# Kernel optimization log

Measured on AMD Instinct MI355X. Metric: run time of the kernel, lower is better.

Reference implementation:

```python
import jax, jax.numpy as jnp
import numpy as np

IN_DIM, UNITS, OUT_DIM = 128, 256, 8
DENSITY = 0.5  # 1 - sparsity_level
B, T = 256, 512


def _ncp_dims():
    Nm = OUT_DIM
    Nc = max(int(0.4 * (UNITS - Nm)), 1)   # command neurons (AutoNCP rule)
    Ni = UNITS - Nm - Nc                    # inter neurons
    return Ni, Nc, Nm


def _fanout_mask(rng, n_src, n_dst, fanout):
    # each source connects to `fanout` distinct random destinations
    idx = np.argsort(rng.random((n_src, n_dst)), axis=1)[:, :fanout]
    m = np.zeros((n_src, n_dst), dtype=np.int32)
    m[np.arange(n_src)[:, None], idx] = 1
    return m


def setup_inputs() -> dict:
    key = jax.random.key(0)
    rng = np.random.default_rng(22222)
    Ni, Nc, Nm = _ncp_dims()
    s_fan = max(int(Ni * DENSITY), 1)       # sensory fanout
    i_fan = max(int(Nc * DENSITY), 1)       # inter fanout
    m_fanin = max(int(Nc * DENSITY), 1)     # motor fanin
    M_si = _fanout_mask(rng, IN_DIM, Ni, s_fan)      # sensory -> inter
    M_ic = _fanout_mask(rng, Ni, Nc, i_fan)          # inter -> command
    M_cm = _fanout_mask(rng, Nm, Nc, m_fanin).T      # command -> motor (fanin per motor)

    def layer_mask(M_in, hid):
        # WiredCfCCell: concat input sparsity with dense ones for the recurrent block, then transpose
        return np.concatenate([M_in, np.ones((hid, hid), np.int32)], axis=0).T

    masks = [layer_mask(M_si, Ni), layer_mask(M_ic, Nc), layer_mask(M_cm, Nm)]
    dims = [(IN_DIM, Ni), (Ni, Nc), (Nc, Nm)]
    inp = {}
    for l, (fin, hid) in enumerate(dims):
        cat = fin + hid
        scale = 1.0 / np.sqrt(cat)
        for nm in ("w1", "w2", "wa", "wb"):
            inp[f"{nm}_{l}"] = jnp.asarray(rng.normal(0.0, scale, (hid, cat)).astype(np.float32))
        for nm in ("b1", "b2", "ba", "bb"):
            inp[f"{nm}_{l}"] = jnp.zeros((hid,), jnp.float32)
        inp[f"m{l}"] = jnp.asarray(masks[l])  # int32, constant sparsity mask
    k1, k2 = jax.random.split(key)
    inp["x"] = jax.random.normal(k1, (B, T, IN_DIM), jnp.float32)
    inp["dt"] = jax.random.uniform(k2, (1,), jnp.float32, 0.5, 1.5)
    return inp


def _cfc_cell(xh, w1, b1, w2, b2, wa, ba, wb, bb, m, ts):
    # CfCCell, mode='default', no backbone, sparsity mask on ff1/ff2 weights
    mf = m.astype(w1.dtype)
    ff1 = jnp.tanh(xh @ (w1 * mf).T + b1)
    ff2 = jnp.tanh(xh @ (w2 * mf).T + b2)
    t_interp = jax.nn.sigmoid((xh @ wa.T + ba) * ts + (xh @ wb.T + bb))
    return ff1 * (1.0 - t_interp) + t_interp * ff2


def _forward(x, dt, params, masks):
    Ni, Nc, Nm = _ncp_dims()
    ts = dt[0]
    h0 = jnp.zeros((x.shape[0], Ni), x.dtype)
    h1 = jnp.zeros((x.shape[0], Nc), x.dtype)
    h2 = jnp.zeros((x.shape[0], Nm), x.dtype)
    p0, p1, p2 = params

    def step(carry, xt):
        h0, h1, h2 = carry
        nh0 = _cfc_cell(jnp.concatenate([xt, h0], 1), *p0, masks[0], ts)
        nh1 = _cfc_cell(jnp.concatenate([nh0, h1], 1), *p1, masks[1], ts)
        nh2 = _cfc_cell(jnp.concatenate([nh1, h2], 1), *p2, masks[2], ts)
        return (nh0, nh1, nh2), nh2

    (h0, h1, h2), ys = jax.lax.scan(step, (h0, h1, h2), jnp.swapaxes(x, 0, 1))
    y = jnp.tanh(jnp.swapaxes(ys, 0, 1))          # (B, T, OUT_DIM), tanh output saturation
    h_out = jnp.concatenate([h0, h1, h2], axis=1)  # (B, units)
    return y, h_out


def reference(x, dt,
              w1_0, b1_0, w2_0, b2_0, wa_0, ba_0, wb_0, bb_0, m0,
              w1_1, b1_1, w2_1, b2_1, wa_1, ba_1, wb_1, bb_1, m1,
              w1_2, b1_2, w2_2, b2_2, wa_2, ba_2, wb_2, bb_2, m2):
    params = ((w1_0, b1_0, w2_0, b2_0, wa_0, ba_0, wb_0, bb_0),
              (w1_1, b1_1, w2_1, b2_1, wa_1, ba_1, wb_1, bb_1),
              (w1_2, b1_2, w2_2, b2_2, wa_2, ba_2, wb_2, bb_2))
    return _forward(x, dt, params, (m0, m1, m2))
```

## Files before the change

kernel.cpp:

```cpp
#include <hip/hip_runtime.h>
#include <cmath>


typedef _Float16 f16;
typedef f16 h4 __attribute__((ext_vector_type(4)));
typedef f16 h8 __attribute__((ext_vector_type(8)));
typedef float f4 __attribute__((ext_vector_type(4)));

#define MFMA(a, b, c) __builtin_amdgcn_mfma_f32_16x16x32_f16(a, b, c, 0, 0, 0)
#define RAW_BAR() asm volatile("s_waitcnt lgkmcnt(0)\n\ts_barrier" ::: "memory")

constexpr int IN_DIM = 128, Ni = 149, Nc = 99, Nm = 8;
constexpr int CAT0 = 277, CAT1 = 248, CAT2 = 107;
constexpr int Bsz = 256, Tsz = 512;
constexpr int TC = 64, NCH = 8, NBT = 16;
constexpr int NT0 = 30, NT1 = 21;
constexpr int S0 = 168, S2 = 136;
constexpr int NXWG1 = 64;
constexpr int NXWG0 = 128;
constexpr size_t XU0C = (size_t)TC * NBT * NT0 * 256;
constexpr size_t NH0C = (size_t)TC * NBT * 2560;
constexpr size_t XU1C = (size_t)TC * NBT * NT1 * 256;
constexpr size_t H0S_HALVES = (size_t)NBT * 16 * S0;
constexpr size_t H12S_HALVES = (size_t)NBT * 2 * 16 * S2;
constexpr size_t YOFF = (size_t)Bsz * Tsz * 8;

constexpr int OFF_X0 = 0;
constexpr int OFF_R0 = 7680;
constexpr int OFF_X1 = 17280;
constexpr int OFF_R12A = 24000;
constexpr int OFF_R12B = 29376;
constexpr int NFRAG = 30144;

__device__ inline float rcpf_(float x) { return __builtin_amdgcn_rcpf(x); }
__device__ __forceinline__ float cfc_h(float a0, float a1, float a2) {
  float e0 = __expf(a0), e1 = __expf(a1), e2 = __expf(a2);
  float pa = 1.f + e0, ma = 1.f - e0;
  float pb = 1.f + e1, mb = 1.f - e1;
  float pc = 1.f + e2;
  float num = fmaf(ma * pb, e2, mb * pa);
  return num * rcpf_(pa * pb * pc);
}
__device__ __forceinline__ float tanhp_(float x) {
  float e = __expf(-2.f * x);
  return (1.f - e) * rcpf_(1.f + e);
}

__global__ __launch_bounds__(256) void pack_kernel(
    const float* __restrict__ w1_0, const float* __restrict__ w2_0,
    const float* __restrict__ wa_0, const float* __restrict__ wb_0,
    const int* __restrict__ m0,
    const float* __restrict__ w1_1, const float* __restrict__ w2_1,
    const float* __restrict__ wa_1, const float* __restrict__ wb_1,
    const int* __restrict__ m1,
    const float* __restrict__ w1_2, const float* __restrict__ w2_2,
    const float* __restrict__ wa_2, const float* __restrict__ wb_2,
    const int* __restrict__ m2, const float* __restrict__ dtp,
    f16* __restrict__ PK) {
  int idx = blockIdx.x * 256 + threadIdx.x;
  if (idx >= NFRAG) return;
  int lane = idx & 63, col = lane & 15, q = lane >> 4;
  float ts = dtp[0];
  const float* Wa = nullptr;
  const float* Wb = nullptr;
  const int* M = nullptr;
  int ld, n, nmax, k0, kmax;
  int mat;
  if (idx < OFF_R0) {
    int p = idx >> 6;
    mat = p / 40; int nt = (p >> 2) % 10, kt = p & 3;
    ld = CAT0; n = nt * 16 + col; nmax = Ni; k0 = kt * 32 + q * 8; kmax = IN_DIM;
    if (mat == 0) { Wa = w1_0; M = m0; }
    else if (mat == 1) { Wa = w2_0; M = m0; }
    else { Wa = wa_0; Wb = wb_0; }
  } else if (idx < OFF_X1) {
    int p = (idx - OFF_R0) >> 6;
    int g = p / 15; mat = (p / 5) % 3; int kt = p % 5;
    ld = CAT0; n = g * 16 + col; nmax = Ni; k0 = IN_DIM + kt * 32 + q * 8; kmax = CAT0;
    if (mat == 0) Wa = w1_0;
    else if (mat == 1) Wa = w2_0;
    else { Wa = wa_0; Wb = wb_0; }
  } else if (idx < OFF_R12A) {
    int p = (idx - OFF_X1) >> 6;
    mat = p / 35; int nt = (p / 5) % 7, kt = p % 5;
    ld = CAT1; n = nt * 16 + col; nmax = Nc; k0 = kt * 32 + q * 8; kmax = Ni;
    if (mat == 0) { Wa = w1_1; M = m1; }
    else if (mat == 1) { Wa = w2_1; M = m1; }
    else { Wa = wa_1; Wb = wb_1; }
  } else if (idx < OFF_R12B) {
    int p = (idx - OFF_R12A) >> 6;
    int wv = p / 12; mat = (p / 4) % 3; int kt = p & 3;
    ld = CAT1; n = wv * 16 + col; nmax = Nc; k0 = Ni + kt * 32 + q * 8; kmax = CAT1;
    if (mat == 0) Wa = w1_1;
    else if (mat == 1) Wa = w2_1;
    else { Wa = wa_1; Wb = wb_1; }
  } else {
    int p = (idx - OFF_R12B) >> 6;
    mat = p / 4; int kt = p & 3;
    ld = CAT2; n = col; nmax = Nm; k0 = kt * 32 + q * 8; kmax = CAT2;
    if (mat == 0) { Wa = w1_2; M = m2; }
    else if (mat == 1) { Wa = w2_2; M = m2; }
    else { Wa = wa_2; Wb = wb_2; }
  }
  h8 r;
#pragma unroll
  for (int j = 0; j < 8; j++) {
    int k = k0 + j;
    float v = 0.f;
    if (n < nmax && k < kmax) {
      if (mat < 2) {
        v = Wa[(size_t)n * ld + k];
        if (M) v *= (float)M[(size_t)n * ld + k];
        v *= -2.f;
      } else {
        v = -(ts * Wa[(size_t)n * ld + k] + Wb[(size_t)n * ld + k]);
      }
    }
    r[j] = (f16)v;
  }
  ((h8*)PK)[idx] = r;
}

__device__ __forceinline__ void r0_step(
    const f16* br, f16* bw, const f16* __restrict__ XU0, f16* __restrict__ NH0,
    float* __restrict__ out, const h8 (&Bf)[3][5], h4 (&xu)[3],
    int t, int tload, int bt, int g, int lane, int col, int q, int n, bool last) {
  h8 A[5];
#pragma unroll
  for (int kt = 0; kt < 5; kt++)
    A[kt] = *(const h8*)(br + col * S0 + kt * 32 + q * 8);
  f4 acc0 = {(float)xu[0][0], (float)xu[0][1], (float)xu[0][2], (float)xu[0][3]};
  f4 acc1 = {(float)xu[1][0], (float)xu[1][1], (float)xu[1][2], (float)xu[1][3]};
  f4 acc2 = {(float)xu[2][0], (float)xu[2][1], (float)xu[2][2], (float)xu[2][3]};
  size_t mtl = (size_t)tload * NBT + bt;
#pragma unroll
  for (int mat = 0; mat < 3; mat++)
    xu[mat] = *(const h4*)(XU0 + (mtl * NT0 + mat * 10 + g) * 256 + lane * 4);
#pragma unroll
  for (int kt = 0; kt < 5; kt++) {
    acc0 = MFMA(A[kt], Bf[0][kt], acc0);
    acc1 = MFMA(A[kt], Bf[1][kt], acc1);
    acc2 = MFMA(A[kt], Bf[2][kt], acc2);
  }
  int mt = t * NBT + bt;
  f16* nh = NH0 + (size_t)mt * 2560;
#pragma unroll
  for (int r = 0; r < 4; r++) {
    int m = q * 4 + r;
    float h = cfc_h(acc0[r], acc1[r], acc2[r]);
    f16 h16 = (f16)h;
    bw[m * S0 + n] = h16;
    nh[m * 160 + n] = h16;
    if (last && n < Ni) out[YOFF + (size_t)(bt * 16 + m) * 256 + n] = h;
  }
}

__device__ __forceinline__ void r12l1_step(
    const f16* br, f16* bw, const f16* __restrict__ XU1, float* __restrict__ out,
    const h8 (&Bf)[3][4], h4 (&xu)[3],
    int tload, int bt, int w, int lane, int col, int q, int n, bool last) {
  h8 A[4];
#pragma unroll
  for (int kt = 0; kt < 4; kt++)
    A[kt] = *(const h8*)(br + col * S2 + kt * 32 + q * 8);
  f4 acc0 = {(float)xu[0][0], (float)xu[0][1], (float)xu[0][2], (float)xu[0][3]};
  f4 acc1 = {(float)xu[1][0], (float)xu[1][1], (float)xu[1][2], (float)xu[1][3]};
  f4 acc2 = {(float)xu[2][0], (float)xu[2][1], (float)xu[2][2], (float)xu[2][3]};
  size_t mtl = (size_t)tload * NBT + bt;
#pragma unroll
  for (int mat = 0; mat < 3; mat++)
    xu[mat] = *(const h4*)(XU1 + (mtl * NT1 + mat * 7 + w) * 256 + lane * 4);
#pragma unroll
  for (int kt = 0; kt < 4; kt++) {
    acc0 = MFMA(A[kt], Bf[0][kt], acc0);
    acc1 = MFMA(A[kt], Bf[1][kt], acc1);
    acc2 = MFMA(A[kt], Bf[2][kt], acc2);
  }
#pragma unroll
  for (int r = 0; r < 4; r++) {
    int m = q * 4 + r;
    float h = cfc_h(acc0[r], acc1[r], acc2[r]);
    if (n < Nc) {
      bw[m * S2 + n] = (f16)h;
      if (last) out[YOFF + (size_t)(bt * 16 + m) * 256 + Ni + n] = h;
    }
  }
}

__device__ __forceinline__ void r12l2_step(
    const f16* rb, f16* wb, float* __restrict__ out, const h8 (&Bf)[3][4],
    float bn0, float bn1, float bn2, int tg, int bt, int col, int q, bool last) {
  h8 A[4];
#pragma unroll
  for (int kt = 0; kt < 4; kt++)
    A[kt] = *(const h8*)(rb + col * S2 + kt * 32 + q * 8);
  f4 acc0 = {bn0, bn0, bn0, bn0};
  f4 acc1 = {bn1, bn1, bn1, bn1};
  f4 acc2 = {bn2, bn2, bn2, bn2};
#pragma unroll
  for (int kt = 0; kt < 4; kt++) {
    acc0 = MFMA(A[kt], Bf[0][kt], acc0);
    acc1 = MFMA(A[kt], Bf[1][kt], acc1);
    acc2 = MFMA(A[kt], Bf[2][kt], acc2);
  }
#pragma unroll
  for (int r = 0; r < 4; r++) {
    int m = q * 4 + r;
    float h = cfc_h(acc0[r], acc1[r], acc2[r]);
    if (col < Nm) {
      out[((size_t)(bt * 16 + m) * Tsz + tg) * 8 + col] = tanhp_(h);
      wb[m * S2 + Nc + col] = (f16)h;
      if (last) out[YOFF + (size_t)(bt * 16 + m) * 256 + Ni + Nc + col] = h;
    }
  }
}

__global__ __launch_bounds__(640) void R_kernel(
    const h8* __restrict__ pk,
    const float* __restrict__ b1_0, const float* __restrict__ b2_0,
    const float* __restrict__ ba_0, const float* __restrict__ bb_0,
    const float* __restrict__ b1_1, const float* __restrict__ b2_1,
    const float* __restrict__ ba_1, const float* __restrict__ bb_1,
    const float* __restrict__ c1, const float* __restrict__ c2,
    const float* __restrict__ ca, const float* __restrict__ cb,
    const float* __restrict__ dtp, const float* __restrict__ x,
    f16* __restrict__ XU0, f16* __restrict__ NH0, f16* __restrict__ XU1,
    f16* __restrict__ H0S, f16* __restrict__ H12S,
    float* __restrict__ out, int c) {
  __shared__ __align__(16) char smem[10752];
  int tid = threadIdx.x;
  int g = tid >> 6, lane = tid & 63, col = lane & 15, q = lane >> 4;
  int wg = blockIdx.x;
  float ts = dtp[0];

  if (wg < NBT) {
    if (c < 0 || c >= NCH) return;
    const f16* XU0r = XU0 + (size_t)(c & 1) * XU0C;
    f16* NH0w = NH0 + (size_t)(c & 1) * NH0C;
    f16(*buf)[16 * S0] = (f16(*)[16 * S0])smem;
    int bt = wg;
    int n = g * 16 + col;
    h8 Bf[3][5];
#pragma unroll
    for (int mat = 0; mat < 3; mat++)
#pragma unroll
      for (int kt = 0; kt < 5; kt++)
        Bf[mat][kt] = pk[OFF_R0 + ((g * 3 + mat) * 5 + kt) * 64 + lane];

    for (int idx = tid; idx < 16 * S0; idx += 640) {
      buf[0][idx] = (c == 0) ? (f16)0.f : H0S[(size_t)bt * 16 * S0 + idx];
      buf[1][idx] = (f16)0.f;
    }
    __syncthreads();

    h4 xu0[3], xu1[3], xu2[3], xu3[3];
#pragma unroll
    for (int mat = 0; mat < 3; mat++) {
      xu0[mat] = *(const h4*)(XU0r + ((size_t)(0 * NBT + bt) * NT0 + mat * 10 + g) * 256 + lane * 4);
      xu1[mat] = *(const h4*)(XU0r + ((size_t)(1 * NBT + bt) * NT0 + mat * 10 + g) * 256 + lane * 4);
      xu2[mat] = *(const h4*)(XU0r + ((size_t)(2 * NBT + bt) * NT0 + mat * 10 + g) * 256 + lane * 4);
      xu3[mat] = *(const h4*)(XU0r + ((size_t)(3 * NBT + bt) * NT0 + mat * 10 + g) * 256 + lane * 4);
    }

    for (int t = 0; t < TC; t += 4) {
      r0_step(buf[0], buf[1], XU0r, NH0w, out, Bf, xu0, t, (t + 4 < TC) ? t + 4 : t,
              bt, g, lane, col, q, n, false);
      RAW_BAR();
      r0_step(buf[1], buf[0], XU0r, NH0w, out, Bf, xu1, t + 1,
              (t + 5 < TC) ? t + 5 : t + 1, bt, g, lane, col, q, n, false);
      RAW_BAR();
      r0_step(buf[0], buf[1], XU0r, NH0w, out, Bf, xu2, t + 2,
              (t + 6 < TC) ? t + 6 : t + 2, bt, g, lane, col, q, n, false);
      RAW_BAR();
      bool lastD = (c == NCH - 1) && (t + 3 == TC - 1);
      r0_step(buf[1], buf[0], XU0r, NH0w, out, Bf, xu3, t + 3,
              (t + 7 < TC) ? t + 7 : t + 3, bt, g, lane, col, q, n, lastD);
      RAW_BAR();
    }
    for (int idx = tid; idx < 16 * S0; idx += 640)
      H0S[(size_t)bt * 16 * S0 + idx] = buf[0][idx];

  } else if (wg < 2 * NBT) {
    int cc = c - 2;
    if (cc < 0 || cc >= NCH) return;
    const f16* XU1r = XU1 + (size_t)(cc & 1) * XU1C;
    f16(*buf)[16 * S2] = (f16(*)[16 * S2])smem;
    int bt = wg - NBT;
    int w = g;
    int n = w * 16 + col;
    h8 Bf[3][4];
    float bn0 = 0.f, bn1 = 0.f, bn2 = 0.f;
    if (w < 7) {
#pragma unroll
      for (int mat = 0; mat < 3; mat++)
#pragma unroll
        for (int kt = 0; kt < 4; kt++)
          Bf[mat][kt] = pk[OFF_R12A + ((w * 3 + mat) * 4 + kt) * 64 + lane];
    } else if (w == 7) {
#pragma unroll
      for (int mat = 0; mat < 3; mat++)
#pragma unroll
        for (int kt = 0; kt < 4; kt++)
          Bf[mat][kt] = pk[OFF_R12B + (mat * 4 + kt) * 64 + lane];
      bn0 = (col < Nm) ? -2.f * c1[col] : 0.f;
      bn1 = (col < Nm) ? -2.f * c2[col] : 0.f;
      bn2 = (col < Nm) ? -(ts * ca[col] + cb[col]) : 0.f;
    }
    for (int idx = tid; idx < 2 * 16 * S2; idx += 640)
      ((f16*)buf)[idx] = (cc == 0) ? (f16)0.f : H12S[(size_t)bt * 2 * 16 * S2 + idx];
    __syncthreads();

    h4 xuA[3], xuB[3];
    if (w < 7) {
#pragma unroll
      for (int mat = 0; mat < 3; mat++) {
        xuA[mat] = *(const h4*)(XU1r + ((size_t)bt * NT1 + mat * 7 + w) * 256 + lane * 4);
        xuB[mat] = *(const h4*)(XU1r +
                                ((size_t)(NBT + bt) * NT1 + mat * 7 + w) * 256 + lane * 4);
      }
    }

    for (int t = 0; t < TC; t += 2) {
      if (w < 7) {
        int tlA = (t + 2 < TC) ? t + 2 : t;
        r12l1_step(buf[0], buf[1], XU1r, out, Bf, xuA, tlA, bt, w, lane, col, q, n,
                   false);
      }
      RAW_BAR();
      if (w == 7)
        r12l2_step(buf[1], buf[0], out, Bf, bn0, bn1, bn2, cc * TC + t, bt, col, q,
                   false);
      if (w < 7) {
        int tlB = (t + 3 < TC) ? t + 3 : t + 1;
        bool lastB = (cc == NCH - 1) && (t + 1 == TC - 1);
        r12l1_step(buf[1], buf[0], XU1r, out, Bf, xuB, tlB, bt, w, lane, col, q, n,
                   lastB);
      }
      RAW_BAR();
      if (w == 7)
        r12l2_step(buf[0], buf[1], out, Bf, bn0, bn1, bn2, cc * TC + t + 1, bt, col, q,
                   (cc == NCH - 1) && (t + 1 == TC - 1));
    }
    __syncthreads();
    for (int idx = tid; idx < 2 * 16 * S2; idx += 640)
      H12S[(size_t)bt * 2 * 16 * S2 + idx] = ((f16*)buf)[idx];

  } else if (wg < 2 * NBT + NXWG1) {
    int cx = c - 1;
    if (cx < 0 || cx >= NCH) return;
    int w = g;
    if (w >= 7) return;
    const f16* NH0r = NH0 + (size_t)(cx & 1) * NH0C;
    f16* XU1w = XU1 + (size_t)(cx & 1) * XU1C;
    int bx = wg - 2 * NBT;
    int n = w * 16 + col;
    h8 Bf[3][5];
    float bias[3];
#pragma unroll
    for (int mat = 0; mat < 3; mat++)
#pragma unroll
      for (int kt = 0; kt < 5; kt++)
        Bf[mat][kt] = pk[OFF_X1 + (mat * 35 + w * 5 + kt) * 64 + lane];
    bias[0] = (n < Nc) ? -2.f * b1_1[n] : 0.f;
    bias[1] = (n < Nc) ? -2.f * b2_1[n] : 0.f;
    bias[2] = (n < Nc) ? -(ts * ba_1[n] + bb_1[n]) : 0.f;
    for (int i = 0; i < (TC * NBT) / NXWG1; i++) {
      int mt = bx * ((TC * NBT) / NXWG1) + i;
      const f16* Ab = NH0r + (size_t)mt * 2560;
      h8 A[5];
#pragma unroll
      for (int kt = 0; kt < 5; kt++)
        A[kt] = *(const h8*)(Ab + col * 160 + kt * 32 + q * 8);
#pragma unroll
      for (int mat = 0; mat < 3; mat++) {
        float b = bias[mat];
        f4 acc = {b, b, b, b};
#pragma unroll
        for (int kt = 0; kt < 5; kt++) acc = MFMA(A[kt], Bf[mat][kt], acc);
        h4 o;
#pragma unroll
        for (int rr = 0; rr < 4; rr++) o[rr] = (f16)acc[rr];
        *(h4*)(XU1w + ((size_t)mt * NT1 + mat * 7 + w) * 256 + lane * 4) = o;
      }
    }

  } else {
    int cn = c + 1;
    if (cn >= NCH) return;
    f16* XU0w = XU0 + (size_t)(cn & 1) * XU0C;
    f16* stg = (f16*)smem;
    int bx = wg - 2 * NBT - NXWG1;
    int w = g;
    int n = w * 16 + col;
    h8 Bx[3][4];
    float bias[3];
#pragma unroll
    for (int mat = 0; mat < 3; mat++)
#pragma unroll
      for (int kt = 0; kt < 4; kt++)
        Bx[mat][kt] = pk[OFF_X0 + ((mat * 10 + w) * 4 + kt) * 64 + lane];
    bias[0] = (n < Ni) ? -2.f * b1_0[n] : 0.f;
    bias[1] = (n < Ni) ? -2.f * b2_0[n] : 0.f;
    bias[2] = (n < Ni) ? -(ts * ba_0[n] + bb_0[n]) : 0.f;
    for (int i = 0; i < (TC * NBT) / NXWG0; i++) {
      int mt = bx * ((TC * NBT) / NXWG0) + i;
      int tl = mt >> 4, bt = mt & 15;
      int tg = cn * TC + tl;
      if (tid < 256) {
        int sr = tid >> 4, sc = (tid & 15) * 8;
        const float* xp = x + ((size_t)(bt * 16 + sr) * Tsz + tg) * IN_DIM + sc;
        h8 hv;
#pragma unroll
        for (int j = 0; j < 8; j++) hv[j] = (f16)xp[j];
        *(h8*)(stg + sr * 136 + sc) = hv;
      }
      __syncthreads();
      h8 A[4];
#pragma unroll
      for (int kt = 0; kt < 4; kt++)
        A[kt] = *(const h8*)(stg + col * 136 + kt * 32 + q * 8);
#pragma unroll
      for (int mat = 0; mat < 3; mat++) {
        float b = bias[mat];
        f4 acc = {b, b, b, b};
#pragma unroll
        for (int kt = 0; kt < 4; kt++) acc = MFMA(A[kt], Bx[mat][kt], acc);
        h4 o;
#pragma unroll
        for (int rr = 0; rr < 4; rr++) o[rr] = (f16)acc[rr];
        *(h4*)(XU0w + ((size_t)mt * NT0 + mat * 10 + w) * 256 + lane * 4) = o;
      }
      __syncthreads();
    }
  }
}

extern "C" void kernel_launch(void* const* d_in, const int* in_sizes, int n_in,
                              void* d_out, int out_size, void* d_ws, size_t ws_size,
                              hipStream_t stream) {
  const float* w1_0 = (const float*)d_in[0];
  const float* w2_0 = (const float*)d_in[1];
  const float* wa_0 = (const float*)d_in[2];
  const float* wb_0 = (const float*)d_in[3];
  const float* b1_0 = (const float*)d_in[4];
  const float* b2_0 = (const float*)d_in[5];
  const float* ba_0 = (const float*)d_in[6];
  const float* bb_0 = (const float*)d_in[7];
  const int* m0 = (const int*)d_in[8];
  const float* w1_1 = (const float*)d_in[9];
  const float* w2_1 = (const float*)d_in[10];
  const float* wa_1 = (const float*)d_in[11];
  const float* wb_1 = (const float*)d_in[12];
  const float* b1_1 = (const float*)d_in[13];
  const float* b2_1 = (const float*)d_in[14];
  const float* ba_1 = (const float*)d_in[15];
  const float* bb_1 = (const float*)d_in[16];
  const int* m1 = (const int*)d_in[17];
  const float* w1_2 = (const float*)d_in[18];
  const float* w2_2 = (const float*)d_in[19];
  const float* wa_2 = (const float*)d_in[20];
  const float* wb_2 = (const float*)d_in[21];
  const float* c1 = (const float*)d_in[22];
  const float* c2 = (const float*)d_in[23];
  const float* ca = (const float*)d_in[24];
  const float* cb = (const float*)d_in[25];
  const int* m2 = (const int*)d_in[26];
  const float* x = (const float*)d_in[27];
  const float* dt = (const float*)d_in[28];
  float* out = (float*)d_out;

  f16* XU0 = (f16*)d_ws;
  f16* NH0 = XU0 + 2 * XU0C;
  f16* XU1 = NH0 + 2 * NH0C;
  f16* H0S = XU1 + 2 * XU1C;
  f16* H12S = H0S + H0S_HALVES;
  f16* PK = H12S + H12S_HALVES;
  const h8* pk = (const h8*)PK;

  pack_kernel<<<(NFRAG + 255) / 256, 256, 0, stream>>>(
      w1_0, w2_0, wa_0, wb_0, m0, w1_1, w2_1, wa_1, wb_1, m1,
      w1_2, w2_2, wa_2, wb_2, m2, dt, PK);

  for (int c = -1; c <= NCH + 1; c++)
    R_kernel<<<2 * NBT + NXWG1 + NXWG0, 640, 0, stream>>>(
        pk, b1_0, b2_0, ba_0, bb_0, b1_1, b2_1, ba_1, bb_1,
        c1, c2, ca, cb, dt, x, XU0, NH0, XU1, H0S, H12S, out, c);
}
```

Measured before the change: 772.7 us.

## Overlap layer-1 input GEMM with recurrence via in-kernel counters; use exp2 with folded log2e

The layer-1/2 recurrence workgroups now consume XU1 from the same launch that produces it. They spin on a per-chunk atomic counter that the XU1 GEMM workgroups increment, which removes one pipeline stage and one kernel launch from the chunk loop. The log2(e) factor is folded into the packed weights and biases so the activations call the hardware exp2 directly. This relies on producer and consumer workgroups being co-resident, since a bounded spin with sleep could deadlock or stall otherwise. It also adds acquire/release fences.

```diff
diff --git a/kernel.cpp b/kernel.cpp
--- a/kernel.cpp
+++ b/kernel.cpp
@@ -24,6 +24,7 @@
 constexpr size_t H0S_HALVES = (size_t)NBT * 16 * S0;
 constexpr size_t H12S_HALVES = (size_t)NBT * 2 * 16 * S2;
 constexpr size_t YOFF = (size_t)Bsz * Tsz * 8;
+constexpr float L2E = 1.4426950408889634f;
 
 constexpr int OFF_X0 = 0;
 constexpr int OFF_R0 = 7680;
@@ -33,8 +34,15 @@
 constexpr int NFRAG = 30144;
 
 __device__ inline float rcpf_(float x) { return __builtin_amdgcn_rcpf(x); }
+__device__ __forceinline__ float exp2p_(float x) {
+#if __has_builtin(__builtin_amdgcn_exp2f)
+  return __builtin_amdgcn_exp2f(x);
+#else
+  return exp2f(x);
+#endif
+}
 __device__ __forceinline__ float cfc_h(float a0, float a1, float a2) {
-  float e0 = __expf(a0), e1 = __expf(a1), e2 = __expf(a2);
+  float e0 = exp2p_(a0), e1 = exp2p_(a1), e2 = exp2p_(a2);
   float pa = 1.f + e0, ma = 1.f - e0;
   float pb = 1.f + e1, mb = 1.f - e1;
   float pc = 1.f + e2;
@@ -42,7 +50,7 @@
   return num * rcpf_(pa * pb * pc);
 }
 __device__ __forceinline__ float tanhp_(float x) {
-  float e = __expf(-2.f * x);
+  float e = exp2p_(-2.f * L2E * x);
   return (1.f - e) * rcpf_(1.f + e);
 }
 
@@ -56,7 +64,10 @@
     const float* __restrict__ w1_2, const float* __restrict__ w2_2,
     const float* __restrict__ wa_2, const float* __restrict__ wb_2,
     const int* __restrict__ m2, const float* __restrict__ dtp,
-    f16* __restrict__ PK) {
+    f16* __restrict__ PK, int* __restrict__ CNT) {
+  if (blockIdx.x == 0 && threadIdx.x < NCH)
+    __hip_atomic_store(&CNT[threadIdx.x], 0, __ATOMIC_RELAXED,
+                       __HIP_MEMORY_SCOPE_AGENT);
   int idx = blockIdx.x * 256 + threadIdx.x;
   if (idx >= NFRAG) return;
   int lane = idx & 63, col = lane & 15, q = lane >> 4;
@@ -111,9 +122,9 @@
       if (mat < 2) {
         v = Wa[(size_t)n * ld + k];
         if (M) v *= (float)M[(size_t)n * ld + k];
-        v *= -2.f;
+        v *= -2.f * L2E;
       } else {
-        v = -(ts * Wa[(size_t)n * ld + k] + Wb[(size_t)n * ld + k]);
+        v = -L2E * (ts * Wa[(size_t)n * ld + k] + Wb[(size_t)n * ld + k]);
       }
     }
     r[j] = (f16)v;
@@ -226,7 +237,7 @@
     const float* __restrict__ dtp, const float* __restrict__ x,
     f16* __restrict__ XU0, f16* __restrict__ NH0, f16* __restrict__ XU1,
     f16* __restrict__ H0S, f16* __restrict__ H12S,
-    float* __restrict__ out, int c) {
+    int* __restrict__ CNT, float* __restrict__ out, int c) {
   __shared__ __align__(16) char smem[10752];
   int tid = threadIdx.x;
   int g = tid >> 6, lane = tid & 63, col = lane & 15, q = lane >> 4;
@@ -281,7 +292,7 @@
       H0S[(size_t)bt * 16 * S0 + idx] = buf[0][idx];
 
   } else if (wg < 2 * NBT) {
-    int cc = c - 2;
+    int cc = c - 1;
     if (cc < 0 || cc >= NCH) return;
     const f16* XU1r = XU1 + (size_t)(cc & 1) * XU1C;
     f16(*buf)[16 * S2] = (f16(*)[16 * S2])smem;
@@ -302,13 +313,25 @@
 #pragma unroll
         for (int kt = 0; kt < 4; kt++)
           Bf[mat][kt] = pk[OFF_R12B + (mat * 4 + kt) * 64 + lane];
-      bn0 = (col < Nm) ? -2.f * c1[col] : 0.f;
-      bn1 = (col < Nm) ? -2.f * c2[col] : 0.f;
-      bn2 = (col < Nm) ? -(ts * ca[col] + cb[col]) : 0.f;
+      bn0 = (col < Nm) ? -2.f * L2E * c1[col] : 0.f;
+      bn1 = (col < Nm) ? -2.f * L2E * c2[col] : 0.f;
+      bn2 = (col < Nm) ? -L2E * (ts * ca[col] + cb[col]) : 0.f;
     }
     for (int idx = tid; idx < 2 * 16 * S2; idx += 640)
       ((f16*)buf)[idx] = (cc == 0) ? (f16)0.f : H12S[(size_t)bt * 2 * 16 * S2 + idx];
     __syncthreads();
+
+    if (tid == 0) {
+      long it = 0;
+      while (__hip_atomic_load(&CNT[cc], __ATOMIC_RELAXED,
+                               __HIP_MEMORY_SCOPE_AGENT) < NXWG1 &&
+             it < (1L << 28)) {
+        __builtin_amdgcn_s_sleep(8);
+        ++it;
+      }
+    }
+    __syncthreads();
+    __builtin_amdgcn_fence(__ATOMIC_ACQUIRE, "agent");
 
     h4 xuA[3], xuB[3];
     if (w < 7) {
@@ -349,40 +372,45 @@
     int cx = c - 1;
     if (cx < 0 || cx >= NCH) return;
     int w = g;
-    if (w >= 7) return;
     const f16* NH0r = NH0 + (size_t)(cx & 1) * NH0C;
     f16* XU1w = XU1 + (size_t)(cx & 1) * XU1C;
     int bx = wg - 2 * NBT;
     int n = w * 16 + col;
-    h8 Bf[3][5];
-    float bias[3];
-#pragma unroll
-    for (int mat = 0; mat < 3; mat++)
-#pragma unroll
-      for (int kt = 0; kt < 5; kt++)
-        Bf[mat][kt] = pk[OFF_X1 + (mat * 35 + w * 5 + kt) * 64 + lane];
-    bias[0] = (n < Nc) ? -2.f * b1_1[n] : 0.f;
-    bias[1] = (n < Nc) ? -2.f * b2_1[n] : 0.f;
-    bias[2] = (n < Nc) ? -(ts * ba_1[n] + bb_1[n]) : 0.f;
-    for (int i = 0; i < (TC * NBT) / NXWG1; i++) {
-      int mt = bx * ((TC * NBT) / NXWG1) + i;
-      const f16* Ab = NH0r + (size_t)mt * 2560;
-      h8 A[5];
-#pragma unroll
-      for (int kt = 0; kt < 5; kt++)
-        A[kt] = *(const h8*)(Ab + col * 160 + kt * 32 + q * 8);
-#pragma unroll
-      for (int mat = 0; mat < 3; mat++) {
-        float b = bias[mat];
-        f4 acc = {b, b, b, b};
-#pragma unroll
-        for (int kt = 0; kt < 5; kt++) acc = MFMA(A[kt], Bf[mat][kt], acc);
-        h4 o;
-#pragma unroll
-        for (int rr = 0; rr < 4; rr++) o[rr] = (f16)acc[rr];
-        *(h4*)(XU1w + ((size_t)mt * NT1 + mat * 7 + w) * 256 + lane * 4) = o;
-      }
-    }
+    if (w < 7) {
+      h8 Bf[3][5];
+      float bias[3];
+#pragma unroll
+      for (int mat = 0; mat < 3; mat++)
+#pragma unroll
+        for (int kt = 0; kt < 5; kt++)
+          Bf[mat][kt] = pk[OFF_X1 + (mat * 35 + w * 5 + kt) * 64 + lane];
+      bias[0] = (n < Nc) ? -2.f * L2E * b1_1[n] : 0.f;
+      bias[1] = (n < Nc) ? -2.f * L2E * b2_1[n] : 0.f;
+      bias[2] = (n < Nc) ? -L2E * (ts * ba_1[n] + bb_1[n]) : 0.f;
+      for (int i = 0; i < (TC * NBT) / NXWG1; i++) {
+        int mt = bx * ((TC * NBT) / NXWG1) + i;
+        const f16* Ab = NH0r + (size_t)mt * 2560;
+        h8 A[5];
+#pragma unroll
+        for (int kt = 0; kt < 5; kt++)
+          A[kt] = *(const h8*)(Ab + col * 160 + kt * 32 + q * 8);
+#pragma unroll
+        for (int mat = 0; mat < 3; mat++) {
+          float b = bias[mat];
+          f4 acc = {b, b, b, b};
+#pragma unroll
+          for (int kt = 0; kt < 5; kt++) acc = MFMA(A[kt], Bf[mat][kt], acc);
+          h4 o;
+#pragma unroll
+          for (int rr = 0; rr < 4; rr++) o[rr] = (f16)acc[rr];
+          *(h4*)(XU1w + ((size_t)mt * NT1 + mat * 7 + w) * 256 + lane * 4) = o;
+        }
+      }
+    }
+    __syncthreads();
+    if (tid == 0)
+      __hip_atomic_fetch_add(&CNT[cx], 1, __ATOMIC_RELEASE,
+                             __HIP_MEMORY_SCOPE_AGENT);
 
   } else {
     int cn = c + 1;
@@ -399,9 +427,9 @@
 #pragma unroll
       for (int kt = 0; kt < 4; kt++)
         Bx[mat][kt] = pk[OFF_X0 + ((mat * 10 + w) * 4 + kt) * 64 + lane];
-    bias[0] = (n < Ni) ? -2.f * b1_0[n] : 0.f;
-    bias[1] = (n < Ni) ? -2.f * b2_0[n] : 0.f;
-    bias[2] = (n < Ni) ? -(ts * ba_0[n] + bb_0[n]) : 0.f;
+    bias[0] = (n < Ni) ? -2.f * L2E * b1_0[n] : 0.f;
+    bias[1] = (n < Ni) ? -2.f * L2E * b2_0[n] : 0.f;
+    bias[2] = (n < Ni) ? -L2E * (ts * ba_0[n] + bb_0[n]) : 0.f;
     for (int i = 0; i < (TC * NBT) / NXWG0; i++) {
       int mt = bx * ((TC * NBT) / NXWG0) + i;
       int tl = mt >> 4, bt = mt & 15;
@@ -475,14 +503,15 @@
   f16* H0S = XU1 + 2 * XU1C;
   f16* H12S = H0S + H0S_HALVES;
   f16* PK = H12S + H12S_HALVES;
+  int* CNT = (int*)(PK + (size_t)NFRAG * 8);
   const h8* pk = (const h8*)PK;
 
   pack_kernel<<<(NFRAG + 255) / 256, 256, 0, stream>>>(
       w1_0, w2_0, wa_0, wb_0, m0, w1_1, w2_1, wa_1, wb_1, m1,
-      w1_2, w2_2, wa_2, wb_2, m2, dt, PK);
-
-  for (int c = -1; c <= NCH + 1; c++)
+      w1_2, w2_2, wa_2, wb_2, m2, dt, PK, CNT);
+
+  for (int c = -1; c <= NCH; c++)
     R_kernel<<<2 * NBT + NXWG1 + NXWG0, 640, 0, stream>>>(
         pk, b1_0, b2_0, ba_0, bb_0, b1_1, b2_1, ba_1, bb_1,
-        c1, c2, ca, cb, dt, x, XU0, NH0, XU1, H0S, H12S, out, c);
-}
+        c1, c2, ca, cb, dt, x, XU0, NH0, XU1, H0S, H12S, CNT, out, c);
+}
```

Result: faster. 732.8 us (-5.2%).
